# Kernel optimization log

Measured on AMD Instinct MI355X. Metric: run time of the kernel, lower is better.

Reference implementation:

```python
import jax, jax.numpy as jnp
import numpy as np

B, S, E, H = 2, 1024, 1024, 16
Dh = E // H


def setup_inputs() -> dict:
    key = jax.random.key(0)
    ks = jax.random.split(key, 32)
    sc = 1.0 / np.sqrt(E)  # xavier-ish scale
    inp = {}
    names_x = ["x_q_a", "x_q_b", "x_kv_a", "x_kv_b"]
    for i, n in enumerate(names_x):
        inp[n] = jax.random.normal(ks[i], (B, S, E), jnp.float32)
    # causal mask, broadcastable to (B, H, S, S); masked where == 0
    inp["mask"] = jnp.tril(jnp.ones((S, S), jnp.int32))[None, None, :, :]
    inp["layer_theta"] = jnp.float32(0.3)
    inp["thetas_head"] = 0.1 * jax.random.normal(ks[4], (H,), jnp.float32)
    i = 5
    for p in ["q", "k", "v", "o"]:
        inp[p + "_wa"] = sc * jax.random.normal(ks[i], (E, E), jnp.float32); i += 1
        inp[p + "_wb"] = sc * jax.random.normal(ks[i], (E, E), jnp.float32); i += 1
        inp[p + "_ba"] = jnp.zeros((E,), jnp.float32)
        inp[p + "_bb"] = jnp.zeros((E,), jnp.float32)
    return inp


def _qc_dense(xa, xb, wa, wb, ba, bb, j2):
    # F.linear: x @ W.T + b ; j2 is a scalar so (Wb*j2) factors out
    out_a = xa @ wa.T + ba + (xb @ wb.T) * j2
    out_b = xa @ wb.T + bb + xb @ wa.T
    return out_a, out_b


def _shape(x):
    # (B,S,E) -> (B,H,S,Dh)
    return x.reshape(B, S, H, Dh).transpose(0, 2, 1, 3)


def _unshape(x):
    return x.transpose(0, 2, 1, 3).reshape(B, S, E)


def _rope(x):
    # standard rotate-half RoPE on last dim, positions over axis -2
    inv_freq = 1.0 / (10000.0 ** (jnp.arange(0, Dh, 2, dtype=jnp.float32) / Dh))
    ang = jnp.arange(S, dtype=jnp.float32)[:, None] * inv_freq[None, :]  # (S, Dh/2)
    cos = jnp.concatenate([jnp.cos(ang), jnp.cos(ang)], axis=-1)  # (S, Dh)
    sin = jnp.concatenate([jnp.sin(ang), jnp.sin(ang)], axis=-1)
    x1, x2 = x[..., : Dh // 2], x[..., Dh // 2:]
    rot = jnp.concatenate([-x2, x1], axis=-1)
    return x * cos + rot * sin


def reference(x_q_a, x_q_b, x_kv_a, x_kv_b, mask, layer_theta, thetas_head,
              q_wa, q_wb, q_ba, q_bb, k_wa, k_wb, k_ba, k_bb,
              v_wa, v_wb, v_ba, v_bb, o_wa, o_wb, o_ba, o_bb):
    j2 = jnp.sin(2.0 * layer_theta) - 1.0
    qa, qb = _qc_dense(x_q_a, x_q_b, q_wa, q_wb, q_ba, q_bb, j2)
    ka, kb = _qc_dense(x_kv_a, x_kv_b, k_wa, k_wb, k_ba, k_bb, j2)
    va, vb = _qc_dense(x_kv_a, x_kv_b, v_wa, v_wb, v_ba, v_bb, j2)
    qa, qb = _rope(_shape(qa)), _rope(_shape(qb))
    ka, kb = _rope(_shape(ka)), _rope(_shape(kb))
    va, vb = _shape(va), _shape(vb)
    j2h = (jnp.sin(2.0 * thetas_head) - 1.0).reshape(1, H, 1, 1)
    # dual QC score matrices (B,H,S,S)
    s_a = jnp.einsum("bhqd,bhkd->bhqk", qa, ka) + jnp.einsum("bhqd,bhkd->bhqk", qb, kb) * j2h
    s_b = jnp.einsum("bhqd,bhkd->bhqk", qa, kb) + jnp.einsum("bhqd,bhkd->bhqk", qb, ka)
    mag = jnp.sqrt(s_a * s_a + s_b * s_b + 1e-8) / np.sqrt(Dh)
    mag = jnp.where(mask == 0, -1e9, mag)
    attn = jax.nn.softmax(mag, axis=-1)
    out_a = _unshape(jnp.einsum("bhqk,bhkd->bhqd", attn, va))
    out_b = _unshape(jnp.einsum("bhqk,bhkd->bhqd", attn, vb))
    return _qc_dense(out_a, out_b, o_wa, o_wb, o_ba, o_bb, j2)
```

## Files before the change

kernel.cpp:

```cpp
#include <hip/hip_runtime.h>
#include <math.h>
#include <stdint.h>

#define BATCH 2
#define SEQ   1024
#define EMB   1024
#define NH    16
#define DH    64
#define BSE   (BATCH*SEQ*EMB)
#define MROWS (BATCH*SEQ)

typedef unsigned short u16;
typedef __attribute__((ext_vector_type(8))) short short8;
typedef __attribute__((ext_vector_type(4))) float f32x4;

__device__ __forceinline__ float bf2f(u16 u) {
    return __uint_as_float(((unsigned int)u) << 16);
}
__device__ __forceinline__ u16 f2bf(float f) {
    unsigned int x = __float_as_uint(f);
    x += 0x7FFFu + ((x >> 16) & 1u);
    return (u16)(x >> 16);
}

__device__ __forceinline__ void async_copy16(const void* g, void* l) {
    __builtin_amdgcn_global_load_lds(
        (const __attribute__((address_space(1))) unsigned int*)g,
        (__attribute__((address_space(3))) unsigned int*)l,
        16, 0, 0);
}

#define VMCNT(N)  asm volatile("s_waitcnt vmcnt(" #N ")" ::: "memory")
#define BARRIER_SYNC() do { asm volatile("" ::: "memory"); \
                            __builtin_amdgcn_s_barrier();  \
                            asm volatile("" ::: "memory"); } while (0)

struct PackArgs {
    const float* src[20];
    u16*         dst[20];
    int          scaled[20];
};

__global__ __launch_bounds__(256) void pack_kernel(PackArgs pa, const float* __restrict__ theta)
{
    const int e = blockIdx.y;
    const size_t i = ((size_t)blockIdx.x * 256 + threadIdx.x) * 4;
    float sc = 1.0f;
    if (pa.scaled[e]) sc = sinf(2.0f * theta[0]) - 1.0f;
    float4 v = *(const float4*)(pa.src[e] + i);
    ushort4 o;
    o.x = f2bf(v.x * sc); o.y = f2bf(v.y * sc);
    o.z = f2bf(v.z * sc); o.w = f2bf(v.w * sc);
    *(ushort4*)(pa.dst[e] + i) = o;
}

struct Gemm8Args {
    const u16*   A1s[6];
    const u16*   A2s[6];
    const u16*   Blo[6];
    const u16*   Bhi[6];
    const float* bias[6];
    void*        dst[6];
    int          mode[6];
};

__global__ __launch_bounds__(512, 2) void mfma_gemm8(Gemm8Args ga)
{
    __shared__ u16 lds[2][2][256][64];

    const int t    = threadIdx.x;
    const int lane = t & 63;
    const int w    = t >> 6;
    const int wm   = w >> 2;
    const int wn   = w & 3;
    const int L15  = lane & 15;
    const int quad = lane >> 4;
    const int rswz = L15 & 7;

    const int bid = blockIdx.x;
    const int xcd = bid & 7;
    const int idx = bid >> 3;
    const int nt  = xcd * 3 + (idx >> 3);
    const int mt  = idx & 7;
    const int m0   = mt * 256;
    const int seg  = nt >> 2;
    const int nloc = (nt & 3) * 256;

    const char* A1 = (const char*)ga.A1s[seg];
    const char* A2 = (const char*)ga.A2s[seg];
    const char* Bl = (const char*)ga.Blo[seg];
    const char* Bh = (const char*)ga.Bhi[seg];

    const int   srow8 = t >> 3;
    const int   g16   = (((t & 7) ^ (srow8 & 7)) << 4);
    const char* A1t = A1 + (size_t)(m0   + srow8) * 2048 + g16;
    const char* A2t = A2 + (size_t)(m0   + srow8) * 2048 + g16;
    const char* Blt = Bl + (size_t)(nloc + srow8) * 2048 + g16;
    const char* Bht = Bh + (size_t)(nloc + srow8) * 2048 + g16;
    char* ldsW = (char*)&lds[0][0][0][0] + w * 1024;

    auto stage_half = [&](int buf, int mat, const char* srcT, size_t kcol, int r0) {
        #pragma unroll
        for (int c = 0; c < 2; ++c)
            async_copy16(srcT + (size_t)(r0 + c*64) * 2048 + kcol,
                         ldsW + buf*65536 + mat*32768 + (r0 + c*64)*128);
    };

    auto ldA = [&](const u16* Abw, int mq, int m, int ks) -> short8 {
        return *(const short8*)(Abw + (mq*128 + m*16)*64 + (((ks*4 + quad) ^ rswz) << 3));
    };
    auto ldB = [&](const u16* Bbw, int nq, int n, int ks) -> short8 {
        return *(const short8*)(Bbw + (nq*128 + n*16)*64 + (((ks*4 + quad) ^ rswz) << 3));
    };

    f32x4 acc00[4][2] = {};
    f32x4 acc01[4][2] = {};
    f32x4 acc11[4][2] = {};
    f32x4 acc10[4][2] = {};
    short8 fa[4][2];
    short8 fb0[2][2];
    short8 fb1[2][2];

    auto mfma4x2 = [&](f32x4 (&accq)[4][2], short8 (&a)[4][2], short8 (&b)[2][2]) {
        __builtin_amdgcn_s_setprio(1);
        #pragma unroll
        for (int m = 0; m < 4; ++m)
            #pragma unroll
            for (int n = 0; n < 2; ++n) {
                accq[m][n] = __builtin_amdgcn_mfma_f32_16x16x32_bf16(a[m][0], b[n][0], accq[m][n], 0, 0, 0);
                accq[m][n] = __builtin_amdgcn_mfma_f32_16x16x32_bf16(a[m][1], b[n][1], accq[m][n], 0, 0, 0);
            }
        __builtin_amdgcn_s_setprio(0);
    };

    stage_half(0, 0, A1t, 0, 0);
    stage_half(0, 1, Blt, 0, 0);
    stage_half(0, 1, Blt, 0, 128);
    stage_half(0, 0, A1t, 0, 128);

    for (int kt = 0; kt < 31; ++kt) {
        const int cur = kt & 1, nxt = cur ^ 1;
        const bool hi = ((kt + 1) & 16) != 0;
        const char* At = hi ? A2t : A1t;
        const char* Bt = hi ? Bht : Blt;
        const size_t kc = (size_t)((kt + 1) & 15) * 128;
        const u16* Abw = &lds[cur][0][wm*64 + L15][0];
        const u16* Bbw = &lds[cur][1][wn*32 + L15][0];

        stage_half(nxt, 0, At, kc, 0);
        VMCNT(6);
        BARRIER_SYNC();
        #pragma unroll
        for (int m = 0; m < 4; ++m)
            #pragma unroll
            for (int ks = 0; ks < 2; ++ks)
                fa[m][ks] = ldA(Abw, 0, m, ks);
        #pragma unroll
        for (int n = 0; n < 2; ++n)
            #pragma unroll
            for (int ks = 0; ks < 2; ++ks)
                fb0[n][ks] = ldB(Bbw, 0, n, ks);
        mfma4x2(acc00, fa, fb0);

        stage_half(nxt, 1, Bt, kc, 0);
        VMCNT(6);
        BARRIER_SYNC();
        #pragma unroll
        for (int n = 0; n < 2; ++n)
            #pragma unroll
            for (int ks = 0; ks < 2; ++ks)
                fb1[n][ks] = ldB(Bbw, 1, n, ks);
        mfma4x2(acc01, fa, fb1);

        stage_half(nxt, 1, Bt, kc, 128);
        VMCNT(6);
        BARRIER_SYNC();
        #pragma unroll
        for (int m = 0; m < 4; ++m)
            #pragma unroll
            for (int ks = 0; ks < 2; ++ks)
                fa[m][ks] = ldA(Abw, 1, m, ks);
        mfma4x2(acc11, fa, fb1);

        stage_half(nxt, 0, At, kc, 128);
        mfma4x2(acc10, fa, fb0);
    }

    {
        const u16* Abw = &lds[1][0][wm*64 + L15][0];
        const u16* Bbw = &lds[1][1][wn*32 + L15][0];

        VMCNT(4);
        BARRIER_SYNC();
        #pragma unroll
        for (int m = 0; m < 4; ++m)
            #pragma unroll
            for (int ks = 0; ks < 2; ++ks)
                fa[m][ks] = ldA(Abw, 0, m, ks);
        #pragma unroll
        for (int n = 0; n < 2; ++n)
            #pragma unroll
            for (int ks = 0; ks < 2; ++ks)
                fb0[n][ks] = ldB(Bbw, 0, n, ks);
        mfma4x2(acc00, fa, fb0);

        VMCNT(2);
        BARRIER_SYNC();
        #pragma unroll
        for (int n = 0; n < 2; ++n)
            #pragma unroll
            for (int ks = 0; ks < 2; ++ks)
                fb1[n][ks] = ldB(Bbw, 1, n, ks);
        mfma4x2(acc01, fa, fb1);

        VMCNT(0);
        BARRIER_SYNC();
        #pragma unroll
        for (int m = 0; m < 4; ++m)
            #pragma unroll
            for (int ks = 0; ks < 2; ++ks)
                fa[m][ks] = ldA(Abw, 1, m, ks);
        mfma4x2(acc11, fa, fb1);

        mfma4x2(acc10, fa, fb0);
    }

    const float* bias = ga.bias[seg];
    const int mode = ga.mode[seg];
    u16* dst = (u16*)ga.dst[seg];

    auto store_quad = [&](f32x4 (&accq)[4][2], int mq, int nq) {
        #pragma unroll
        for (int n = 0; n < 2; ++n) {
            const int c = nloc + nq*128 + wn*32 + n*16 + L15;
            const float bv = bias[c];
            #pragma unroll
            for (int m = 0; m < 4; ++m) {
                #pragma unroll
                for (int reg = 0; reg < 4; ++reg) {
                    const int row = m0 + mq*128 + wm*64 + m*16 + quad*4 + reg;
                    const float val = accq[m][n][reg] + bv;
                    if (mode == 2) {
                        dst[((size_t)(row >> 10) << 20) + (size_t)c*1024 + (row & 1023)] = f2bf(val);
                    } else {
                        dst[(size_t)row*1024 + c] = f2bf(val);
                    }
                }
            }
        }
    };
    store_quad(acc00, 0, 0);
    store_quad(acc01, 0, 1);
    store_quad(acc11, 1, 1);
    store_quad(acc10, 1, 0);
}

struct GemmArgs {
    const u16*   A1s[8];
    const u16*   A2s[8];
    const u16*   Blo[8];
    const u16*   Bhi[8];
    const float* bias[8];
    void*        dst[8];
    int          mode[8];
};

template<int SPLITK>
__global__ __launch_bounds__(256) void mfma_gemm(GemmArgs ga)
{
    __shared__ u16 sA[128][32];
    __shared__ u16 sB[128][32];

    const int t    = threadIdx.x;
    const int lane = t & 63;
    const int w    = t >> 6;
    const int wx   = w & 1;
    const int wy   = w >> 1;
    const int n0   = blockIdx.y * 128;
    const int m0   = blockIdx.x * 128;
    const int ko   = (SPLITK == 2) ? blockIdx.z : 0;
    const int seg  = n0 >> 10;
    const int nloc = n0 & 1023;

    const int srow = t >> 2;
    const int sb   = (t & 3) * 16;

    f32x4 acc[4][4] = {};

    const char* A1 = (const char*)ga.A1s[seg];
    const char* A2 = (const char*)ga.A2s[seg];
    const char* Bl = (const char*)ga.Blo[seg];
    const char* Bh = (const char*)ga.Bhi[seg];
    if (SPLITK == 2 && ko) { A1 = A2; Bl = Bh; }

    const int frow = lane & 15;
    const int quad = lane >> 4;

    const int NKT = (SPLITK == 2) ? 32 : 64;
    for (int kt = 0; kt < NKT; ++kt) {
        const char* As = (SPLITK == 1 && (kt & 32)) ? A2 : A1;
        const char* Bs = (SPLITK == 1 && (kt & 32)) ? Bh : Bl;
        const size_t kbyte = (size_t)(kt & 31) * 64;

        __syncthreads();
        #pragma unroll
        for (int r = 0; r < 2; ++r) {
            const int row = r*64 + srow;
            const int ldsoff = (r*64 + w*16) * 64;
            async_copy16(As + (size_t)(m0 + row)*2048 + kbyte + sb,
                         (char*)&sA[0][0] + ldsoff);
            async_copy16(Bs + (size_t)(nloc + row)*2048 + kbyte + sb,
                         (char*)&sB[0][0] + ldsoff);
        }
        __syncthreads();

        short8 af[4], bfr[4];
        #pragma unroll
        for (int i = 0; i < 4; ++i)
            af[i] = *(const short8*)&sA[wy*64 + i*16 + frow][quad*8];
        #pragma unroll
        for (int j = 0; j < 4; ++j)
            bfr[j] = *(const short8*)&sB[wx*64 + j*16 + frow][quad*8];

        #pragma unroll
        for (int i = 0; i < 4; ++i)
            #pragma unroll
            for (int j = 0; j < 4; ++j)
                acc[i][j] = __builtin_amdgcn_mfma_f32_16x16x32_bf16(
                                af[i], bfr[j], acc[i][j], 0, 0, 0);
    }

    const float* bias = ga.bias[seg];
    const int mode = ga.mode[seg];

    #pragma unroll
    for (int j = 0; j < 4; ++j) {
        const int c = nloc + wx*64 + j*16 + frow;
        const float bv = (SPLITK == 2 && ko) ? 0.0f : bias[c];
        #pragma unroll
        for (int i = 0; i < 4; ++i) {
            #pragma unroll
            for (int reg = 0; reg < 4; ++reg) {
                const int m = m0 + wy*64 + i*16 + quad*4 + reg;
                const float val = acc[i][j][reg] + bv;
                if (mode == 1) {
                    if (SPLITK == 2)
                        atomicAdd((float*)ga.dst[seg] + (size_t)m*1024 + c, val);
                    else
                        ((float*)ga.dst[seg])[(size_t)m*1024 + c] = val;
                } else if (mode == 2) {
                    ((u16*)ga.dst[seg])[((size_t)(m >> 10) << 20) + (size_t)c*1024 + (m & 1023)] = f2bf(val);
                } else {
                    ((u16*)ga.dst[seg])[(size_t)m*1024 + c] = f2bf(val);
                }
            }
        }
    }
}

__global__ __launch_bounds__(256) void rope_kernel(
    u16* qa, u16* qb, u16* ka, u16* kb)
{
    u16* p;
    switch (blockIdx.y) {
        case 0:  p = qa; break;
        case 1:  p = qb; break;
        case 2:  p = ka; break;
        default: p = kb; break;
    }
    const int i   = blockIdx.x * 256 + threadIdx.x;
    const int d   = i & 31;
    const int hh  = (i >> 5) & (NH - 1);
    const int row = i >> 9;
    const int s   = row & (SEQ - 1);
    const size_t base = (size_t)row * EMB + hh * DH;

    float x1 = bf2f(p[base + d]);
    float x2 = bf2f(p[base + d + 32]);
    const float invf_rev = expf(-(float)d * 0.28782313662425576f) * 0.15915494309189535f;
    float rev = (float)s * invf_rev;
    rev -= floorf(rev);
    const float sn = __builtin_amdgcn_sinf(rev);
    const float cs = __builtin_amdgcn_cosf(rev);
    p[base + d]      = f2bf(x1 * cs - x2 * sn);
    p[base + d + 32] = f2bf(x2 * cs + x1 * sn);
}

__global__ __launch_bounds__(256) void attn_mfma(
    const u16* __restrict__ qa, const u16* __restrict__ qb,
    const u16* __restrict__ ka, const u16* __restrict__ kb,
    const u16* __restrict__ vat, const u16* __restrict__ vbt,
    const float* __restrict__ thetas,
    u16* __restrict__ oa, u16* __restrict__ ob)
{
    __shared__ u16 sKa[64][64];
    __shared__ u16 sKb[64][64];
    __shared__ u16 sVa[64][64];
    __shared__ u16 sVb[64][64];
    __shared__ u16 sP[4][16][72];

    const int t    = threadIdx.x;
    const int lane = t & 63;
    const int w    = t >> 6;
    const int L15  = lane & 15;
    const int quad = lane >> 4;

    const int bid  = blockIdx.x;
    const int aa   = (bid >> 5) & 7;
    const int qt   = (bid >> 8) ? aa : (15 - aa);
    const int bh   = bid & 31;
    const int h    = bh & 15;
    const int b    = bh >> 4;

    const float j2h = sinf(2.0f * thetas[h]) - 1.0f;

    const int   qrow  = qt*64 + w*16 + L15;
    const size_t qbase = (size_t)(b*SEQ + qrow) * EMB + h*DH;
    short8 fqa[2], fqb[2], fjqb[2];
    fqa[0] = *(const short8*)(qa + qbase + quad*8);
    fqa[1] = *(const short8*)(qa + qbase + 32 + quad*8);
    fqb[0] = *(const short8*)(qb + qbase + quad*8);
    fqb[1] = *(const short8*)(qb + qbase + 32 + quad*8);
    #pragma unroll
    for (int s2 = 0; s2 < 2; ++s2) {
        short8 src = fqb[s2], dst;
        #pragma unroll
        for (int j = 0; j < 8; ++j)
            dst[j] = (short)f2bf(bf2f((u16)src[j]) * j2h);
        fjqb[s2] = dst;
    }

    f32x4 acc_a[4] = {};
    f32x4 acc_b[4] = {};
    float l_lane[4] = {0.f, 0.f, 0.f, 0.f};

    const int subrow = lane >> 3;
    const int g      = (lane & 7) ^ subrow;
    const int swz    = L15 & 7;

    for (int kt = 0; kt <= qt; ++kt) {
        __syncthreads();
        #pragma unroll
        for (int i = 0; i < 2; ++i) {
            const int row = w*16 + i*8 + subrow;
            const int ldsoff = (w*16 + i*8) * 128;
            const size_t ktok = (size_t)(b*SEQ + kt*64 + row);
            async_copy16((const char*)ka + ktok*2048 + h*128 + g*16,
                         (char*)&sKa[0][0] + ldsoff);
            async_copy16((const char*)kb + ktok*2048 + h*128 + g*16,
                         (char*)&sKb[0][0] + ldsoff);
            const size_t vrow = (size_t)b*1048576 + (size_t)(h*64 + row)*1024 + kt*64;
            async_copy16((const char*)vat + vrow*2 + g*16,
                         (char*)&sVa[0][0] + ldsoff);
            async_copy16((const char*)vbt + vrow*2 + g*16,
                         (char*)&sVb[0][0] + ldsoff);
        }
        __syncthreads();

        f32x4 sa[4] = {}, sb[4] = {};
        #pragma unroll
        for (int n = 0; n < 4; ++n) {
            const u16* rKa = &sKa[n*16 + L15][0];
            const u16* rKb = &sKb[n*16 + L15][0];
            short8 ka0 = *(const short8*)(rKa + (( quad      ^ swz) << 3));
            short8 ka1 = *(const short8*)(rKa + (((4 + quad) ^ swz) << 3));
            short8 kb0 = *(const short8*)(rKb + (( quad      ^ swz) << 3));
            short8 kb1 = *(const short8*)(rKb + (((4 + quad) ^ swz) << 3));
            sa[n] = __builtin_amdgcn_mfma_f32_16x16x32_bf16(fqa[0],  ka0, sa[n], 0, 0, 0);
            sa[n] = __builtin_amdgcn_mfma_f32_16x16x32_bf16(fqa[1],  ka1, sa[n], 0, 0, 0);
            sa[n] = __builtin_amdgcn_mfma_f32_16x16x32_bf16(fjqb[0], kb0, sa[n], 0, 0, 0);
            sa[n] = __builtin_amdgcn_mfma_f32_16x16x32_bf16(fjqb[1], kb1, sa[n], 0, 0, 0);
            sb[n] = __builtin_amdgcn_mfma_f32_16x16x32_bf16(fqa[0],  kb0, sb[n], 0, 0, 0);
            sb[n] = __builtin_amdgcn_mfma_f32_16x16x32_bf16(fqa[1],  kb1, sb[n], 0, 0, 0);
            sb[n] = __builtin_amdgcn_mfma_f32_16x16x32_bf16(fqb[0],  ka0, sb[n], 0, 0, 0);
            sb[n] = __builtin_amdgcn_mfma_f32_16x16x32_bf16(fqb[1],  ka1, sb[n], 0, 0, 0);
        }

        float p[4][4];
        if (kt == qt) {
            #pragma unroll
            for (int n = 0; n < 4; ++n)
                #pragma unroll
                for (int r = 0; r < 4; ++r) {
                    const float A = sa[n][r], B = sb[n][r];
                    const float mag = __builtin_amdgcn_sqrtf(A*A + B*B + 1e-8f) * 0.125f;
                    const bool masked = (n*16 + L15) > (w*16 + quad*4 + r);
                    p[n][r] = masked ? 0.0f
                                     : __builtin_amdgcn_exp2f(mag * 1.44269504f);
                }
        } else {
            #pragma unroll
            for (int n = 0; n < 4; ++n)
                #pragma unroll
                for (int r = 0; r < 4; ++r) {
                    const float A = sa[n][r], B = sb[n][r];
                    const float mag = __builtin_amdgcn_sqrtf(A*A + B*B + 1e-8f) * 0.125f;
                    p[n][r] = __builtin_amdgcn_exp2f(mag * 1.44269504f);
                }
        }
        #pragma unroll
        for (int r = 0; r < 4; ++r)
            l_lane[r] += (p[0][r] + p[1][r]) + (p[2][r] + p[3][r]);

        #pragma unroll
        for (int n = 0; n < 4; ++n)
            #pragma unroll
            for (int r = 0; r < 4; ++r)
                sP[w][quad*4 + r][n*16 + L15] = f2bf(p[n][r]);

        short8 pf0 = *(const short8*)&sP[w][L15][quad*8];
        short8 pf1 = *(const short8*)&sP[w][L15][32 + quad*8];

        #pragma unroll
        for (int n = 0; n < 4; ++n) {
            const u16* rVa = &sVa[n*16 + L15][0];
            const u16* rVb = &sVb[n*16 + L15][0];
            short8 va0 = *(const short8*)(rVa + (( quad      ^ swz) << 3));
            short8 va1 = *(const short8*)(rVa + (((4 + quad) ^ swz) << 3));
            short8 vb0 = *(const short8*)(rVb + (( quad      ^ swz) << 3));
            short8 vb1 = *(const short8*)(rVb + (((4 + quad) ^ swz) << 3));
            acc_a[n] = __builtin_amdgcn_mfma_f32_16x16x32_bf16(pf0, va0, acc_a[n], 0, 0, 0);
            acc_a[n] = __builtin_amdgcn_mfma_f32_16x16x32_bf16(pf1, va1, acc_a[n], 0, 0, 0);
            acc_b[n] = __builtin_amdgcn_mfma_f32_16x16x32_bf16(pf0, vb0, acc_b[n], 0, 0, 0);
            acc_b[n] = __builtin_amdgcn_mfma_f32_16x16x32_bf16(pf1, vb1, acc_b[n], 0, 0, 0);
        }
    }

    float inv[4];
    #pragma unroll
    for (int r = 0; r < 4; ++r) {
        float l = l_lane[r];
        #pragma unroll
        for (int off = 8; off >= 1; off >>= 1)
            l += __shfl_xor(l, off, 64);
        inv[r] = 1.0f / l;
    }

    #pragma unroll
    for (int reg = 0; reg < 4; ++reg) {
        const size_t tok = (size_t)(b*SEQ + qt*64 + w*16 + quad*4 + reg);
        #pragma unroll
        for (int n = 0; n < 4; ++n) {
            const size_t idx = tok*EMB + h*DH + n*16 + L15;
            oa[idx] = f2bf(acc_a[n][reg] * inv[reg]);
            ob[idx] = f2bf(acc_b[n][reg] * inv[reg]);
        }
    }
}

extern "C" void kernel_launch(void* const* d_in, const int* in_sizes, int n_in,
                              void* d_out, int out_size, void* d_ws, size_t ws_size,
                              hipStream_t stream)
{
    const float* x_q_a  = (const float*)d_in[0];
    const float* x_q_b  = (const float*)d_in[1];
    const float* x_kv_a = (const float*)d_in[2];
    const float* x_kv_b = (const float*)d_in[3];
    const float* theta    = (const float*)d_in[5];
    const float* thetas_h = (const float*)d_in[6];
    const float* q_wa = (const float*)d_in[7];
    const float* q_wb = (const float*)d_in[8];
    const float* q_ba = (const float*)d_in[9];
    const float* q_bb = (const float*)d_in[10];
    const float* k_wa = (const float*)d_in[11];
    const float* k_wb = (const float*)d_in[12];
    const float* k_ba = (const float*)d_in[13];
    const float* k_bb = (const float*)d_in[14];
    const float* v_wa = (const float*)d_in[15];
    const float* v_wb = (const float*)d_in[16];
    const float* v_ba = (const float*)d_in[17];
    const float* v_bb = (const float*)d_in[18];
    const float* o_wa = (const float*)d_in[19];
    const float* o_wb = (const float*)d_in[20];
    const float* o_ba = (const float*)d_in[21];
    const float* o_bb = (const float*)d_in[22];

    u16* W = (u16*)d_ws;
    const size_t XN = (size_t)BSE;
    const size_t WN = (size_t)EMB*EMB;
    u16* xq_a16  = W;
    u16* xq_b16  = W + XN;
    u16* xkv_a16 = W + 2*XN;
    u16* xkv_b16 = W + 3*XN;
    u16* wbase   = W + 4*XN;
    u16* q_wa16  = wbase;
    u16* q_wb16  = wbase + WN;
    u16* k_wa16  = wbase + 2*WN;
    u16* k_wb16  = wbase + 3*WN;
    u16* v_wa16  = wbase + 4*WN;
    u16* v_wb16  = wbase + 5*WN;
    u16* o_wa16  = wbase + 6*WN;
    u16* o_wb16  = wbase + 7*WN;
    u16* q_wbs16 = wbase + 8*WN;
    u16* k_wbs16 = wbase + 9*WN;
    u16* v_wbs16 = wbase + 10*WN;
    u16* o_wbs16 = wbase + 11*WN;
    u16* qkv     = wbase + 12*WN;
    u16* qa16 = qkv;
    u16* qb16 = qkv + XN;
    u16* ka16 = qkv + 2*XN;
    u16* kb16 = qkv + 3*XN;
    u16* vat16 = qkv + 4*XN;
    u16* vbt16 = qkv + 5*XN;
    u16* ao16 = xq_a16;
    u16* bo16 = xq_b16;

    float* out_a = (float*)d_out;
    float* out_b = out_a + (size_t)BSE;

    PackArgs pa;
    int si = 0;
    auto add = [&](const float* s, u16* d, int scaled, int chunks) {
        for (int c = 0; c < chunks; ++c) {
            pa.src[si] = s + (size_t)c * WN;
            pa.dst[si] = d + (size_t)c * WN;
            pa.scaled[si] = scaled;
            ++si;
        }
    };
    add(x_q_a,  xq_a16,  0, 2);
    add(x_q_b,  xq_b16,  0, 2);
    add(x_kv_a, xkv_a16, 0, 2);
    add(x_kv_b, xkv_b16, 0, 2);
    add(q_wa, q_wa16, 0, 1);  add(q_wb, q_wb16, 0, 1);
    add(k_wa, k_wa16, 0, 1);  add(k_wb, k_wb16, 0, 1);
    add(v_wa, v_wa16, 0, 1);  add(v_wb, v_wb16, 0, 1);
    add(o_wa, o_wa16, 0, 1);  add(o_wb, o_wb16, 0, 1);
    add(q_wb, q_wbs16, 1, 1); add(k_wb, k_wbs16, 1, 1);
    add(v_wb, v_wbs16, 1, 1); add(o_wb, o_wbs16, 1, 1);
    pack_kernel<<<dim3(WN/1024, 20), 256, 0, stream>>>(pa, theta);

    hipMemsetAsync(d_out, 0, (size_t)out_size * sizeof(float), stream);

    Gemm8Args g8;
    {
        const u16* a1s[6] = { xq_a16, xq_a16, xkv_a16, xkv_a16, xkv_a16, xkv_a16 };
        const u16* a2s[6] = { xq_b16, xq_b16, xkv_b16, xkv_b16, xkv_b16, xkv_b16 };
        const u16* blo[6] = { q_wa16, q_wb16, k_wa16, k_wb16, v_wa16, v_wb16 };
        const u16* bhi[6] = { q_wbs16, q_wa16, k_wbs16, k_wa16, v_wbs16, v_wa16 };
        const float* bia[6] = { q_ba, q_bb, k_ba, k_bb, v_ba, v_bb };
        void* dsts[6] = { qa16, qb16, ka16, kb16, vat16, vbt16 };
        const int modes[6] = { 0, 0, 0, 0, 2, 2 };
        for (int s = 0; s < 6; ++s) {
            g8.A1s[s] = a1s[s]; g8.A2s[s] = a2s[s];
            g8.Blo[s] = blo[s]; g8.Bhi[s] = bhi[s];
            g8.bias[s] = bia[s]; g8.dst[s] = dsts[s]; g8.mode[s] = modes[s];
        }
    }
    mfma_gemm8<<<dim3(192), 512, 0, stream>>>(g8);

    rope_kernel<<<dim3((BATCH*SEQ*NH*32)/256, 4), 256, 0, stream>>>(qa16, qb16, ka16, kb16);

    attn_mfma<<<BATCH*NH*(SEQ/64), 256, 0, stream>>>(qa16, qb16, ka16, kb16,
                                                     vat16, vbt16, thetas_h, ao16, bo16);

    GemmArgs g3;
    for (int s = 0; s < 8; ++s) {
        g3.A1s[s] = ao16; g3.A2s[s] = bo16;
        g3.Blo[s] = o_wa16; g3.Bhi[s] = o_wbs16;
        g3.bias[s] = o_ba; g3.dst[s] = out_a; g3.mode[s] = 1;
    }
    g3.Blo[1] = o_wb16; g3.Bhi[1] = o_wa16; g3.bias[1] = o_bb; g3.dst[1] = out_b;
    mfma_gemm<2><<<dim3(MROWS/128, 16, 2), 256, 0, stream>>>(g3);
}
```

Baseline: 313.5 us.

## Reorder GEMM k-loop so LDS fragment reads overlap async global-to-LDS staging

Restructures the double-buffered GEMM main loop so each quadrant's LDS fragment reads are issued before the next async global->LDS stage and the barrier. Explicit lgkmcnt(0) waits with sched_barrier then gate the MFMA blocks. This moves the barrier and vmcnt points so the LDS read latency and barrier wait hide behind in-flight global loads. The risk is a subtle race if the staging halves overwrite LDS regions still being read, and the added sched_barriers limit compiler interleaving.

Measured after the change: 312.7 us. About the same (-0.3%).

```diff
diff --git a/kernel.cpp b/kernel.cpp
--- a/kernel.cpp
+++ b/kernel.cpp
@@ -34,6 +34,8 @@
 #define BARRIER_SYNC() do { asm volatile("" ::: "memory"); \
                             __builtin_amdgcn_s_barrier();  \
                             asm volatile("" ::: "memory"); } while (0)
+#define LGKM0() do { asm volatile("s_waitcnt lgkmcnt(0)" ::: "memory"); \
+                     __builtin_amdgcn_sched_barrier(0); } while (0)
 
 struct PackArgs {
     const float* src[20];
@@ -121,6 +123,21 @@
     short8 fb0[2][2];
     short8 fb1[2][2];
 
+    auto readA = [&](const u16* Abw, int mq) {
+        #pragma unroll
+        for (int m = 0; m < 4; ++m)
+            #pragma unroll
+            for (int ks = 0; ks < 2; ++ks)
+                fa[m][ks] = ldA(Abw, mq, m, ks);
+    };
+    auto readB = [&](const u16* Bbw, int nq, short8 (&fb)[2][2]) {
+        #pragma unroll
+        for (int n = 0; n < 2; ++n)
+            #pragma unroll
+            for (int ks = 0; ks < 2; ++ks)
+                fb[n][ks] = ldB(Bbw, nq, n, ks);
+    };
+
     auto mfma4x2 = [&](f32x4 (&accq)[4][2], short8 (&a)[4][2], short8 (&b)[2][2]) {
         __builtin_amdgcn_s_setprio(1);
         #pragma unroll
@@ -137,6 +154,8 @@
     stage_half(0, 1, Blt, 0, 0);
     stage_half(0, 1, Blt, 0, 128);
     stage_half(0, 0, A1t, 0, 128);
+    VMCNT(4);
+    BARRIER_SYNC();
 
     for (int kt = 0; kt < 31; ++kt) {
         const int cur = kt & 1, nxt = cur ^ 1;
@@ -147,42 +166,29 @@
         const u16* Abw = &lds[cur][0][wm*64 + L15][0];
         const u16* Bbw = &lds[cur][1][wn*32 + L15][0];
 
+        readA(Abw, 0);
+        readB(Bbw, 0, fb0);
         stage_half(nxt, 0, At, kc, 0);
-        VMCNT(6);
-        BARRIER_SYNC();
-        #pragma unroll
-        for (int m = 0; m < 4; ++m)
-            #pragma unroll
-            for (int ks = 0; ks < 2; ++ks)
-                fa[m][ks] = ldA(Abw, 0, m, ks);
-        #pragma unroll
-        for (int n = 0; n < 2; ++n)
-            #pragma unroll
-            for (int ks = 0; ks < 2; ++ks)
-                fb0[n][ks] = ldB(Bbw, 0, n, ks);
-        mfma4x2(acc00, fa, fb0);
-
         stage_half(nxt, 1, Bt, kc, 0);
         VMCNT(6);
         BARRIER_SYNC();
-        #pragma unroll
-        for (int n = 0; n < 2; ++n)
-            #pragma unroll
-            for (int ks = 0; ks < 2; ++ks)
-                fb1[n][ks] = ldB(Bbw, 1, n, ks);
-        mfma4x2(acc01, fa, fb1);
-
+        LGKM0();
+        mfma4x2(acc00, fa, fb0);
+
+        readB(Bbw, 1, fb1);
         stage_half(nxt, 1, Bt, kc, 128);
         VMCNT(6);
         BARRIER_SYNC();
-        #pragma unroll
-        for (int m = 0; m < 4; ++m)
-            #pragma unroll
-            for (int ks = 0; ks < 2; ++ks)
-                fa[m][ks] = ldA(Abw, 1, m, ks);
+        LGKM0();
+        mfma4x2(acc01, fa, fb1);
+
+        readA(Abw, 1);
+        stage_half(nxt, 0, At, kc, 128);
+        VMCNT(4);
+        BARRIER_SYNC();
+        LGKM0();
         mfma4x2(acc11, fa, fb1);
 
-        stage_half(nxt, 0, At, kc, 128);
         mfma4x2(acc10, fa, fb0);
     }
 
@@ -190,38 +196,22 @@
         const u16* Abw = &lds[1][0][wm*64 + L15][0];
         const u16* Bbw = &lds[1][1][wn*32 + L15][0];
 
-        VMCNT(4);
-        BARRIER_SYNC();
-        #pragma unroll
-        for (int m = 0; m < 4; ++m)
-            #pragma unroll
-            for (int ks = 0; ks < 2; ++ks)
-                fa[m][ks] = ldA(Abw, 0, m, ks);
-        #pragma unroll
-        for (int n = 0; n < 2; ++n)
-            #pragma unroll
-            for (int ks = 0; ks < 2; ++ks)
-                fb0[n][ks] = ldB(Bbw, 0, n, ks);
-        mfma4x2(acc00, fa, fb0);
-
+        readA(Abw, 0);
+        readB(Bbw, 0, fb0);
         VMCNT(2);
         BARRIER_SYNC();
-        #pragma unroll
-        for (int n = 0; n < 2; ++n)
-            #pragma unroll
-            for (int ks = 0; ks < 2; ++ks)
-                fb1[n][ks] = ldB(Bbw, 1, n, ks);
-        mfma4x2(acc01, fa, fb1);
-
+        LGKM0();
+        mfma4x2(acc00, fa, fb0);
+
+        readB(Bbw, 1, fb1);
         VMCNT(0);
         BARRIER_SYNC();
-        #pragma unroll
-        for (int m = 0; m < 4; ++m)
-            #pragma unroll
-            for (int ks = 0; ks < 2; ++ks)
-                fa[m][ks] = ldA(Abw, 1, m, ks);
+        LGKM0();
+        mfma4x2(acc01, fa, fb1);
+
+        readA(Abw, 1);
+        LGKM0();
         mfma4x2(acc11, fa, fb1);
-
         mfma4x2(acc10, fa, fb0);
     }
 
```
